# Kernel tuning notes

Hardware: AMD Instinct MI355X
Metric: run time of the kernel (lower is better)

The kernel has to match this reference:

```python
import jax, jax.numpy as jnp
import numpy as np

EPS = 1e-5

def inorm(x, w, b):
    # InstanceNorm1d over token dim (axis=1), per (batch, feature); biased var
    m = x.mean(axis=1, keepdims=True)
    v = ((x - m) ** 2).mean(axis=1, keepdims=True)
    return (x - m) / jnp.sqrt(v + EPS) * w + b

def setup_inputs() -> dict:
    B, N, D, FH = 2, 512, 128, 512
    key = jax.random.key(0)
    ks = iter(jax.random.split(key, 48))
    rn = lambda shape, s=0.05: jax.random.normal(next(ks), shape, jnp.float32) * s
    inp = {
        'row_emb': jax.random.normal(next(ks), (B, N, D), jnp.float32),
        'col_emb': jax.random.normal(next(ks), (B, N, D), jnp.float32),
        'cost_mat': jax.random.uniform(next(ks), (B, N, N), jnp.float32),
        'coords': jax.random.uniform(next(ks), (B, N, 2), jnp.float32),
        'alpha': jnp.ones((1,), jnp.float32),
        # instance norm affine params (weight~1, bias~0)
        'n1_w': 1.0 + rn((D,)), 'n1_b': rn((D,)),
        'n2_w': 1.0 + rn((D,)), 'n2_b': rn((D,)),
        'n3_w': 1.0 + rn((D,)), 'n3_b': rn((D,)),
        'fn1_w': 1.0 + rn((D,)), 'fn1_b': rn((D,)),
        'fn2_w': 1.0 + rn((D,)), 'fn2_b': rn((D,)),
        # AFTFull projections (stored (in,out))
        'q_w': rn((D, D)), 'q_b': rn((D,)),
        'k_w': rn((D, D)), 'k_b': rn((D,)),
        'v_w': rn((D, D)), 'v_b': rn((D,)),
        'p_w': rn((D, D)), 'p_b': rn((D,)),
        'mhc_w': rn((D, D)), 'mhc_b': rn((D,)),
        # DistAngleFusion MLPs
        'dist_w1': rn((1, D)), 'dist_b1': rn((D,)),
        'dist_w2': rn((D, D)), 'dist_b2': rn((D,)),
        'ang_w1': rn((1, D)), 'ang_b1': rn((D,)),
        'ang_w2': rn((D, D)), 'ang_b2': rn((D,)),
        'gate_w': rn((2 * D, 1)), 'gate_b': rn((1,)),
        'outlin_w': rn((D, 1)), 'outlin_b': rn((1,)),
        # FeedForward
        'ffn_w1': rn((D, FH)), 'ffn_b1': rn((FH,)),
        'ffn_w2': rn((FH, D)), 'ffn_b2': rn((D,)),
    }
    return inp

def reference(row_emb, col_emb, cost_mat, coords, alpha,
              n1_w, n1_b, n2_w, n2_b, n3_w, n3_b, fn1_w, fn1_b, fn2_w, fn2_b,
              q_w, q_b, k_w, k_b, v_w, v_b, p_w, p_b, mhc_w, mhc_b,
              dist_w1, dist_b1, dist_w2, dist_b2,
              ang_w1, ang_b1, ang_w2, ang_b2,
              gate_w, gate_b, outlin_w, outlin_b,
              ffn_w1, ffn_b1, ffn_w2, ffn_b2):
    rn = inorm(row_emb, n1_w, n1_b)
    cn = inorm(col_emb, n2_w, n2_b)

    # DistAngleFusion: adapt_bias (B,N,N)
    diff = coords[:, :, None, :] - coords[:, None, :, :]  # (B,N,N,2)
    angles = jnp.arctan2(diff[..., 1], diff[..., 0])
    dist_e = jax.nn.relu(cost_mat[..., None] @ dist_w1 + dist_b1) @ dist_w2 + dist_b2  # (B,N,N,D)
    angle_e = jax.nn.relu(angles[..., None] @ ang_w1 + ang_b1) @ ang_w2 + ang_b2
    g = jax.nn.sigmoid(jnp.concatenate([dist_e, angle_e], axis=-1) @ gate_w + gate_b)  # (B,N,N,1)
    fused = g * dist_e + (1.0 - g) * angle_e
    adapt_bias = (fused @ outlin_w + outlin_b)[..., 0] * alpha  # (B,N,N)

    # AFTFull
    Q = jax.nn.sigmoid(rn @ q_w + q_b)          # (B,N,H)
    K = jax.nn.softmax(cn @ k_w + k_b, axis=1)  # softmax over tokens
    V = cn @ v_w + v_b
    eab = jnp.exp(jax.nn.softmax(adapt_bias, axis=-1))  # (B,N,N)
    eK = jnp.exp(K)
    num = jnp.einsum('bnm,bmh->bnh', eab, eK * V)
    den = jnp.einsum('bnm,bmh->bnh', eab, eK)
    Yt = (Q * (num / den)) @ p_w + p_b

    mh = inorm(Yt @ mhc_w + mhc_b, n3_w, n3_b)

    # TransformerFFN with instance norms
    x = inorm(rn + mh, fn1_w, fn1_b)
    ff = jax.nn.relu(x @ ffn_w1 + ffn_b1) @ ffn_w2 + ffn_b2
    return inorm(x + ff, fn2_w, fn2_b)
```

## Files before the change

### kernel.cpp

```cpp
#include <hip/hip_runtime.h>
#include <hip/hip_bf16.h>
#include <math.h>

#define Bn  2
#define Nn  512
#define Dn  128
#define FHn 512

#define PI_F 3.14159265358979323846f

typedef __hip_bfloat16 bf16;

__device__ __forceinline__ float cvt(float x) { return x; }
__device__ __forceinline__ float cvt(bf16 x) { return __bfloat162float(x); }
__device__ __forceinline__ float sigmoidf_(float x) { return 1.0f / (1.0f + __expf(-x)); }
__device__ __forceinline__ bool is_bf16(const void* alpha) {
    return ((const unsigned short*)alpha)[0] == 0x3F80;
}

__device__ __forceinline__ float fatan2f(float dy, float dx) {
    float ax = fabsf(dx), ay = fabsf(dy);
    float mx = fmaxf(ax, ay), mn = fminf(ax, ay);
    float r = __fdividef(mn, mx);
    float t = r * r;
    float a = r * (0.99997726f + t * (-0.33262347f + t * (0.19354346f +
              t * (-0.11643287f + t * (0.05265332f + t * (-0.01172120f))))));
    if (ay > ax) a = 1.57079632679489662f - a;
    if (dx < 0.f) a = PI_F - a;
    if (dy < 0.f) a = -a;
    return fminf(fmaxf(a, -PI_F), PI_F);
}

#define S_ 131072
#define WS_Q    (0 * S_)
#define WS_K    (1 * S_)
#define WS_V    (2 * S_)
#define WS_EK   (3 * S_)
#define WS_EKV  (4 * S_)
#define WS_EAB  (5 * S_)
#define WS_MH   (1 * S_)
#define WS_T    (2 * S_)
#define WS_OP   (3 * S_)
#define WS_ST   (9 * S_)

#define ST_IN_SC   0
#define ST_IN_SH   512
#define ST_X_SC    2048
#define ST_X_SH    2304
#define ST_PRE     3072
#define P_SC       1024
#define ST_TAB     4224
#define TAB_ANG 644
#define TAB_N   1288
#define ST_LUTC (ST_TAB + TAB_N)
#define ST_LUTA (ST_LUTC + 257)
#define TABLUT_N (TAB_N + 514)

#define SMEM_FLOATS 2568

struct KP {
    const void *row, *col, *cost, *coords, *alpha;
    const void *n1w, *n1b, *n2w, *n2b, *n3w, *n3b, *f1w, *f1b, *f2w, *f2b;
    const void *qw, *qb, *kw, *kb, *vw, *vb, *pw, *pb, *mw, *mb;
    const void *dw1, *db1, *dw2, *db2, *aw1, *ab1, *aw2, *ab2, *gw, *gb, *ow, *ob;
    const void *ffw1, *ffb1, *ffw2, *ffb2;
    void* out;
    float* ws;
};

__device__ __forceinline__ void blk_sum2(float& s, float& ss, volatile float* scr) {
#pragma unroll
    for (int off = 32; off > 0; off >>= 1) { s += __shfl_down(s, off); ss += __shfl_down(ss, off); }
    __syncthreads();
    int wave = threadIdx.x >> 6, lane = threadIdx.x & 63;
    if (lane == 0) { scr[wave] = s; scr[4 + wave] = ss; }
    __syncthreads();
    s = scr[0] + scr[1] + scr[2] + scr[3];
    ss = scr[4] + scr[5] + scr[6] + scr[7];
}

__device__ __forceinline__ float blk_sum1(float v, volatile float* scr) {
#pragma unroll
    for (int off = 32; off > 0; off >>= 1) v += __shfl_down(v, off);
    __syncthreads();
    int wave = threadIdx.x >> 6, lane = threadIdx.x & 63;
    if (lane == 0) scr[wave] = v;
    __syncthreads();
    return scr[0] + scr[1] + scr[2] + scr[3];
}

__device__ __forceinline__ float blk_max1(float v, volatile float* scr) {
#pragma unroll
    for (int off = 32; off > 0; off >>= 1) v = fmaxf(v, __shfl_down(v, off));
    __syncthreads();
    int wave = threadIdx.x >> 6, lane = threadIdx.x & 63;
    if (lane == 0) scr[wave] = v;
    __syncthreads();
    return fmaxf(fmaxf(scr[0], scr[1]), fmaxf(scr[2], scr[3]));
}

template <typename T>
__device__ void build_tables(const T* w1p, const T* b1p, const T* w2p,
                             const T* owp, const T* gwp, float* gtab, float* smem) {
    int tid = threadIdx.x;
    float* W  = smem;
    float* Bb = smem + 128;
    float* U  = smem + 256;
    float* Vv = smem + 384;
    float* Tt = smem + 512;
    int* RK   = (int*)(smem + 640);
    float* STl = smem + 768;
    if (tid < 128) {
        float u = 0.f, v = 0.f;
#pragma unroll 4
        for (int d = 0; d < Dn; ++d) {
            float w2 = cvt(w2p[tid * Dn + d]);
            u += w2 * cvt(owp[d]);
            v += w2 * cvt(gwp[d]);
        }
        float w = cvt(w1p[tid]), b = cvt(b1p[tid]);
        U[tid] = u; Vv[tid] = v; W[tid] = w; Bb[tid] = b;
        Tt[tid] = (w != 0.f) ? (-b / w) : 3.0e38f;
    }
    __syncthreads();
    if (tid < 128) {
        float tk = Tt[tid]; int r = 0;
        for (int j = 0; j < 128; ++j) {
            float tj = Tt[j];
            r += (tj < tk) || (tj == tk && j < tid);
        }
        RK[tid] = r;
        gtab[r] = tk;
        STl[r] = tk;
    }
    __syncthreads();
    if (tid <= 128) {
        int si = tid;
        float slS = 0, inS = 0, slT = 0, inT = 0;
        for (int k = 0; k < 128; ++k) {
            float w = W[k];
            if (w == 0.f) {
                float rb = fmaxf(Bb[k], 0.f);
                inS += rb * U[k];
                inT += rb * Vv[k];
            } else {
                bool act = (w > 0.f) ? (RK[k] < si) : (RK[k] >= si);
                if (act) {
                    slS += w * U[k];  inS += Bb[k] * U[k];
                    slT += w * Vv[k]; inT += Bb[k] * Vv[k];
                }
            }
        }
        gtab[128 + si] = slS;
        gtab[257 + si] = inS;
        gtab[386 + si] = slT;
        gtab[515 + si] = inT;
    }
}

__device__ __forceinline__ int bsearch128(const float* T, float c) {
    int lo = 0, hi = 128;
    while (lo < hi) { int mid = (lo + hi) >> 1; if (T[mid] <= c) lo = mid + 1; else hi = mid; }
    return lo;
}

template <typename T>
__device__ void phase0(const KP& p, float* st, float* smem) {
    float* scr = smem + 2560;
    int cid = blockIdx.x;
    int tid = threadIdx.x;
    {
        int which = cid >> 8, b = (cid >> 7) & 1, d = cid & 127;
        const T* src = (const T*)(which ? p.col : p.row) + (size_t)b * Nn * Dn + d;
        float x0 = cvt(src[(size_t)tid * Dn]);
        float x1 = cvt(src[(size_t)(tid + 256) * Dn]);
        float s = x0 + x1, ss = x0 * x0 + x1 * x1;
        blk_sum2(s, ss, scr);
        if (tid == 0) {
            float m = s * (1.f / Nn);
            float v = fmaxf(ss * (1.f / Nn) - m * m, 0.f);
            float rstd = rsqrtf(v + 1e-5f);
            const T* w = which ? (const T*)p.n2w : (const T*)p.n1w;
            const T* bb = which ? (const T*)p.n2b : (const T*)p.n1b;
            float sc = rstd * cvt(w[d]);
            st[ST_IN_SC + cid] = sc;
            st[ST_IN_SH + cid] = cvt(bb[d]) - m * sc;
        }
    }
    __syncthreads();
    if (cid == 128) {
        const T* db2 = (const T*)p.db2; const T* ab2 = (const T*)p.ab2;
        const T* ow = (const T*)p.ow;   const T* gw = (const T*)p.gw;
        float d2 = 0.f, a2 = 0.f, o = 0.f, g0 = 0.f, g1 = 0.f;
        if (tid < 128) {
            d2 = cvt(db2[tid]); a2 = cvt(ab2[tid]);
            o = cvt(ow[tid]); g0 = cvt(gw[tid]); g1 = cvt(gw[Dn + tid]);
        }
        float cds = d2 * o, cdt = d2 * g0, cas = a2 * o, cat = a2 * g1;
        blk_sum2(cds, cdt, scr);
        blk_sum2(cas, cat, scr);
        if (tid == 0) {
            float* pre = st + ST_PRE;
            pre[P_SC + 0] = cds; pre[P_SC + 1] = cdt;
            pre[P_SC + 2] = cas; pre[P_SC + 3] = cat;
            pre[P_SC + 4] = cvt(((const T*)p.gb)[0]);
            pre[P_SC + 5] = cvt(((const T*)p.ob)[0]);
            pre[P_SC + 6] = cvt(((const T*)p.alpha)[0]);
        }
    } else if (cid == 129) {
        build_tables<T>((const T*)p.dw1, (const T*)p.db1, (const T*)p.dw2,
                        (const T*)p.ow, (const T*)p.gw, st + ST_TAB, smem);
        __syncthreads();
        const float* STl = smem + 768;
        for (int e = tid; e < 257; e += 256) {
            float c = e * (1.f / 256.f);
            st[ST_LUTC + e] = (float)bsearch128(STl, c);
        }
    } else if (cid == 130) {
        build_tables<T>((const T*)p.aw1, (const T*)p.ab1, (const T*)p.aw2,
                        (const T*)p.ow, (const T*)p.gw + Dn, st + ST_TAB + TAB_ANG, smem);
        __syncthreads();
        const float* STl = smem + 768;
        for (int e = tid; e < 257; e += 256) {
            float a = -PI_F + e * (PI_F / 128.f);
            st[ST_LUTA + e] = (float)bsearch128(STl, a);
        }
    }
}

template <typename T>
__device__ void phase1(const KP& p, float* st, float* smem) {
    int tid = threadIdx.x;
    int r0 = blockIdx.x * 2;
    int b = r0 >> 9;
    const T* row = (const T*)p.row; const T* col = (const T*)p.col;
    float* ws = p.ws;
    float* Q = ws + WS_Q; float* Kraw = ws + WS_K; float* V = ws + WS_V;

    float* lr = smem;
    float* lc = smem + 256;
    float* redq = smem + 512;
    float* redk = smem + 1024;
    float* redv = smem + 1536;
    {
        int r = tid >> 7, d = tid & 127;
        float scR = st[ST_IN_SC + b * 128 + d],       shR = st[ST_IN_SH + b * 128 + d];
        float scC = st[ST_IN_SC + 256 + b * 128 + d], shC = st[ST_IN_SH + 256 + b * 128 + d];
        lr[r * 128 + d] = cvt(row[(size_t)(r0 + r) * Dn + d]) * scR + shR;
        lc[r * 128 + d] = cvt(col[(size_t)(r0 + r) * Dn + d]) * scC + shC;
    }
    __syncthreads();
    {
        int h = tid & 127, half = tid >> 7;
        const T* qw = (const T*)p.qw; const T* kw = (const T*)p.kw; const T* vw = (const T*)p.vw;
        float q0 = 0, q1 = 0, ka = 0, kb_ = 0, v0 = 0, v1 = 0;
        int ks = half * 64;
#pragma unroll 8
        for (int k = ks; k < ks + 64; ++k) {
            float wq = cvt(qw[k * Dn + h]);
            float wk = cvt(kw[k * Dn + h]);
            float wv = cvt(vw[k * Dn + h]);
            q0 += lr[k] * wq;        q1 += lr[128 + k] * wq;
            ka += lc[k] * wk;        kb_ += lc[128 + k] * wk;
            v0 += lc[k] * wv;        v1 += lc[128 + k] * wv;
        }
        redq[half * 256 + h] = q0;  redq[half * 256 + 128 + h] = q1;
        redk[half * 256 + h] = ka;  redk[half * 256 + 128 + h] = kb_;
        redv[half * 256 + h] = v0;  redv[half * 256 + 128 + h] = v1;
    }
    __syncthreads();
    if (tid < 128) {
        int h = tid;
        float bq = cvt(((const T*)p.qb)[h]);
        float bk = cvt(((const T*)p.kb)[h]);
        float bv = cvt(((const T*)p.vb)[h]);
#pragma unroll
        for (int r = 0; r < 2; ++r) {
            Q[(r0 + r) * Dn + h]    = sigmoidf_(redq[r * 128 + h] + redq[256 + r * 128 + h] + bq);
            Kraw[(r0 + r) * Dn + h] = redk[r * 128 + h] + redk[256 + r * 128 + h] + bk;
            V[(r0 + r) * Dn + h]    = redv[r * 128 + h] + redv[256 + r * 128 + h] + bv;
        }
    }
    __syncthreads();

    float* tab  = smem;
    float* lutc = smem + 1288;
    float* luta = smem + 1545;
    float* scr  = smem + 1824;
    const float* gt = st + ST_TAB;
    for (int e = tid; e < TABLUT_N; e += 256) smem[e] = gt[e];
    __syncthreads();
    float* eab = ws + WS_EAB;
    const float* pre = st + ST_PRE;
    float cds = pre[P_SC + 0], cdt = pre[P_SC + 1], cas = pre[P_SC + 2], cat = pre[P_SC + 3];
    float gbias = pre[P_SC + 4], obias = pre[P_SC + 5], alpha = pre[P_SC + 6];
    const T* cost = (const T*)p.cost;
    const T* coords = (const T*)p.coords;
    const float* tabA = tab + TAB_ANG;

    float av[2][2];
#pragma unroll
    for (int rr = 0; rr < 2; ++rr) {
        int rowi = r0 + rr;
        int i = rowi & 511;
        float cix = cvt(coords[((size_t)b * Nn + i) * 2 + 0]);
        float ciy = cvt(coords[((size_t)b * Nn + i) * 2 + 1]);
        const T* crow = cost + (size_t)b * Nn * Nn + (size_t)i * Nn;
#pragma unroll
        for (int jj = 0; jj < 2; ++jj) {
            int j = tid + jj * 256;
            float c = cvt(crow[j]);
            int k = (int)(c * 256.f); k = k < 0 ? 0 : (k > 255 ? 255 : k);
            int lo = (int)lutc[k], hi = (int)lutc[k + 1];
            while (lo < hi && tab[lo] <= c) ++lo;
            float sd = fmaf(tab[128 + lo], c, tab[257 + lo]) + cds;
            float td = fmaf(tab[386 + lo], c, tab[515 + lo]) + cdt;
            float dx = cix - cvt(coords[((size_t)b * Nn + j) * 2 + 0]);
            float dy = ciy - cvt(coords[((size_t)b * Nn + j) * 2 + 1]);
            float ang = (dx == 0.f && dy == 0.f) ? 0.f : fatan2f(dy, dx);
            int ka = (int)((ang + PI_F) * (128.f / PI_F)); ka = ka < 0 ? 0 : (ka > 255 ? 255 : ka);
            int la = (int)luta[ka], ha = (int)luta[ka + 1];
            while (la < ha && tabA[la] <= ang) ++la;
            float sa = fmaf(tabA[128 + la], ang, tabA[257 + la]) + cas;
            float ta = fmaf(tabA[386 + la], ang, tabA[515 + la]) + cat;
            float gv = sigmoidf_(td + ta + gbias);
            av[rr][jj] = alpha * (gv * sd + (1.f - gv) * sa + obias);
        }
    }
    int wave = tid >> 6, lane = tid & 63;
    float m0 = fmaxf(av[0][0], av[0][1]);
    float m1 = fmaxf(av[1][0], av[1][1]);
#pragma unroll
    for (int off = 32; off > 0; off >>= 1) {
        m0 = fmaxf(m0, __shfl_down(m0, off));
        m1 = fmaxf(m1, __shfl_down(m1, off));
    }
    if (lane == 0) { scr[wave] = m0; scr[4 + wave] = m1; }
    __syncthreads();
    float mx0 = fmaxf(fmaxf(scr[0], scr[1]), fmaxf(scr[2], scr[3]));
    float mx1 = fmaxf(fmaxf(scr[4], scr[5]), fmaxf(scr[6], scr[7]));
    float e00 = __expf(av[0][0] - mx0), e01 = __expf(av[0][1] - mx0);
    float e10 = __expf(av[1][0] - mx1), e11 = __expf(av[1][1] - mx1);
    float s0 = e00 + e01, s1 = e10 + e11;
#pragma unroll
    for (int off = 32; off > 0; off >>= 1) {
        s0 += __shfl_down(s0, off);
        s1 += __shfl_down(s1, off);
    }
    if (lane == 0) { scr[8 + wave] = s0; scr[12 + wave] = s1; }
    __syncthreads();
    float rs0 = 1.f / (scr[8] + scr[9] + scr[10] + scr[11]);
    float rs1 = 1.f / (scr[12] + scr[13] + scr[14] + scr[15]);
    float* o0 = eab + (size_t)r0 * Nn;
    float* o1 = eab + (size_t)(r0 + 1) * Nn;
    o0[tid] = __expf(e00 * rs0);  o0[tid + 256] = __expf(e01 * rs0);
    o1[tid] = __expf(e10 * rs1);  o1[tid + 256] = __expf(e11 * rs1);
}

__device__ void phase2(const KP& p, float* smem) {
    float* scr = smem + 2560;
    int tid = threadIdx.x;
    int c = blockIdx.x;
    int b = c >> 7, h = c & 127;
    float* ws = p.ws;
    const float* Kraw = ws + WS_K;
    const float* V = ws + WS_V;
    float* eK = ws + WS_EK;
    float* eKV = ws + WS_EKV;
    const float* kb = Kraw + (size_t)b * Nn * Dn + h;
    const float* vb = V + (size_t)b * Nn * Dn + h;
    float x0 = kb[(size_t)tid * Dn];
    float x1 = kb[(size_t)(tid + 256) * Dn];
    float mx = blk_max1(fmaxf(x0, x1), scr);
    float e0 = __expf(x0 - mx), e1 = __expf(x1 - mx);
    float s = blk_sum1(e0 + e1, scr);
    float rs = 1.f / s;
    size_t a0 = (size_t)b * Nn * Dn + (size_t)tid * Dn + h;
    size_t a1 = (size_t)b * Nn * Dn + (size_t)(tid + 256) * Dn + h;
    float ek0 = __expf(e0 * rs), ek1 = __expf(e1 * rs);
    eK[a0] = ek0;  eKV[a0] = ek0 * vb[(size_t)tid * Dn];
    eK[a1] = ek1;  eKV[a1] = ek1 * vb[(size_t)(tid + 256) * Dn];
}

template <typename T>
__device__ void phase3(const KP& p, float* smem) {
    int tid = threadIdx.x;
    int r0 = blockIdx.x * 4;
    int b = r0 >> 9;
    float* ws = p.ws;
    const float* eab = ws + WS_EAB;
    const float* eK = ws + WS_EK;
    const float* eKV = ws + WS_EKV;
    const float* Q = ws + WS_Q;
    float* mh = ws + WS_MH;

    float* ab   = smem;
    float* redn = smem + 2048;
    float* redd = smem + 4096;
    float* gl   = smem + 6144;
    float* yl   = smem + 6656;

    {
        float4* ab4 = (float4*)ab;
        const float4* g4 = (const float4*)(eab + (size_t)r0 * Nn);
        ab4[tid] = g4[tid];
    }
    __syncthreads();
    int h = tid & 127, q = tid >> 7;
    {
        float num[4] = {0,0,0,0}, den[4] = {0,0,0,0};
        int j0 = q * 128;
        const float* ekb = eK + (size_t)b * Nn * Dn + h;
        const float* evb = eKV + (size_t)b * Nn * Dn + h;
#pragma unroll 4
        for (int j = j0; j < j0 + 128; ++j) {
            float ek = ekb[(size_t)j * Dn];
            float ev = evb[(size_t)j * Dn];
#pragma unroll
            for (int r = 0; r < 4; ++r) {
                num[r] += ab[r * 512 + j] * ev;
                den[r] += ab[r * 512 + j] * ek;
            }
        }
#pragma unroll
        for (int r = 0; r < 4; ++r) {
            redn[q * 512 + r * 128 + h] = num[r];
            redd[q * 512 + r * 128 + h] = den[r];
        }
    }
    __syncthreads();
    if (tid < 128) {
#pragma unroll
        for (int r = 0; r < 4; ++r) {
            float nu = redn[r * 128 + h] + redn[512 + r * 128 + h]
                     + redn[1024 + r * 128 + h] + redn[1536 + r * 128 + h];
            float de = redd[r * 128 + h] + redd[512 + r * 128 + h]
                     + redd[1024 + r * 128 + h] + redd[1536 + r * 128 + h];
            gl[r * 128 + h] = Q[(r0 + r) * Dn + h] * nu / de;
        }
    }
    __syncthreads();
    {
        const T* pw = (const T*)p.pw;
        float acc[4] = {0,0,0,0};
        int ks = q * 32;
#pragma unroll 8
        for (int k = ks; k < ks + 32; ++k) {
            float w = cvt(pw[k * Dn + h]);
#pragma unroll
            for (int r = 0; r < 4; ++r) acc[r] += gl[r * 128 + k] * w;
        }
#pragma unroll
        for (int r = 0; r < 4; ++r) redn[q * 512 + r * 128 + h] = acc[r];
    }
    __syncthreads();
    if (tid < 128) {
        float bp = cvt(((const T*)p.pb)[h]);
#pragma unroll
        for (int r = 0; r < 4; ++r)
            yl[r * 128 + h] = redn[r * 128 + h] + redn[512 + r * 128 + h]
                            + redn[1024 + r * 128 + h] + redn[1536 + r * 128 + h] + bp;
    }
    __syncthreads();
    {
        const T* mw = (const T*)p.mw;
        float acc[4] = {0,0,0,0};
        int ks = q * 32;
#pragma unroll 8
        for (int k = ks; k < ks + 32; ++k) {
            float w = cvt(mw[k * Dn + h]);
#pragma unroll
            for (int r = 0; r < 4; ++r) acc[r] += yl[r * 128 + k] * w;
        }
#pragma unroll
        for (int r = 0; r < 4; ++r) redn[q * 512 + r * 128 + h] = acc[r];
    }
    __syncthreads();
    if (tid < 128) {
        float bm = cvt(((const T*)p.mb)[h]);
#pragma unroll
        for (int r = 0; r < 4; ++r)
            mh[(r0 + r) * Dn + h] = redn[r * 128 + h] + redn[512 + r * 128 + h]
                                  + redn[1024 + r * 128 + h] + redn[1536 + r * 128 + h] + bm;
    }
}

template <typename T>
__device__ void phase45(const KP& p, float* st, float* smem) {
    float* scr = smem + 2560;
    int tid = threadIdx.x;
    int c = blockIdx.x;
    int b = c >> 7, d = c & 127;
    const float* mh = p.ws + WS_MH;
    const float* mp = mh + (size_t)b * Nn * Dn + d;
    float m0 = mp[(size_t)tid * Dn], m1 = mp[(size_t)(tid + 256) * Dn];
    float s = m0 + m1, ss = m0 * m0 + m1 * m1;
    blk_sum2(s, ss, scr);
    float mm = s * (1.f / Nn);
    float vv = fmaxf(ss * (1.f / Nn) - mm * mm, 0.f);
    float rstd = rsqrtf(vv + 1e-5f);
    float scM = rstd * cvt(((const T*)p.n3w)[d]);
    float shM = cvt(((const T*)p.n3b)[d]) - mm * scM;
    const T* row = (const T*)p.row;
    float scI = st[ST_IN_SC + c], shI = st[ST_IN_SH + c];
    const T* rp = row + (size_t)b * Nn * Dn + d;
    float* tp = p.ws + WS_T + (size_t)b * Nn * Dn + d;
    float x0 = cvt(rp[(size_t)tid * Dn]) * scI + shI + m0 * scM + shM;
    float x1 = cvt(rp[(size_t)(tid + 256) * Dn]) * scI + shI + m1 * scM + shM;
    tp[(size_t)tid * Dn] = x0;
    tp[(size_t)(tid + 256) * Dn] = x1;
    __syncthreads();
    float s2 = x0 + x1, ss2 = x0 * x0 + x1 * x1;
    blk_sum2(s2, ss2, scr);
    if (tid == 0) {
        float m = s2 * (1.f / Nn);
        float v = fmaxf(ss2 * (1.f / Nn) - m * m, 0.f);
        float r = rsqrtf(v + 1e-5f);
        float sc = r * cvt(((const T*)p.f1w)[d]);
        st[ST_X_SC + c] = sc;
        st[ST_X_SH + c] = cvt(((const T*)p.f1b)[d]) - m * sc;
    }
}

template <typename T>
__device__ void phase6(const KP& p, float* st, float* smem) {
    int tid = threadIdx.x;
    int r0 = blockIdx.x * 4;
    int b = r0 >> 9;
    const float* t = p.ws + WS_T;
    float* outpre = p.ws + WS_OP;
    const T* w1 = (const T*)p.ffw1; const T* b1 = (const T*)p.ffb1;
    const T* w2 = (const T*)p.ffw2; const T* b2 = (const T*)p.ffb2;

    float* xl = smem;
    float* hl = smem + 512;
    float* red = smem + 2560;
    {
        int r = tid >> 7, d = tid & 127;
        int c = b * 128 + d;
        xl[r * 128 + d] = t[(r0 + r) * Dn + d] * st[ST_X_SC + c] + st[ST_X_SH + c];
    }
    __syncthreads();
    {
        int f = tid;
        float a[4] = {0,0,0,0};
#pragma unroll 4
        for (int k = 0; k < Dn; ++k) {
            float w = cvt(w1[k * FHn + f]);
#pragma unroll
            for (int r = 0; r < 4; ++r) a[r] += xl[r * 128 + k] * w;
        }
        float bb1 = cvt(b1[f]);
#pragma unroll
        for (int r = 0; r < 4; ++r) hl[r * 512 + f] = fmaxf(a[r] + bb1, 0.f);
    }
    __syncthreads();
    {
        int d = tid & 127, q = tid >> 7;
        int k0 = q * 128;
        float a[4] = {0,0,0,0};
#pragma unroll 8
        for (int k = k0; k < k0 + 128; ++k) {
            float w = cvt(w2[k * Dn + d]);
#pragma unroll
            for (int r = 0; r < 4; ++r) a[r] += hl[r * 512 + k] * w;
        }
#pragma unroll
        for (int r = 0; r < 4; ++r) red[q * 512 + r * 128 + d] = a[r];
    }
    __syncthreads();
    if (tid < 128) {
        float bb2 = cvt(b2[tid]);
#pragma unroll
        for (int r = 0; r < 4; ++r) {
            float sum = red[r * 128 + tid] + red[512 + r * 128 + tid]
                      + red[1024 + r * 128 + tid] + red[1536 + r * 128 + tid];
            outpre[(r0 + r) * Dn + tid] = xl[r * 128 + tid] + sum + bb2;
        }
    }
}

template <typename T>
__device__ void phase78(const KP& p, float* smem) {
    float* scr = smem + 2560;
    int tid = threadIdx.x;
    int c = blockIdx.x;
    int b = c >> 7, d = c & 127;
    const float* op = p.ws + WS_OP;
    const float* sp = op + (size_t)b * Nn * Dn + d;
    float x0 = sp[(size_t)tid * Dn], x1 = sp[(size_t)(tid + 256) * Dn];
    float s = x0 + x1, ss = x0 * x0 + x1 * x1;
    blk_sum2(s, ss, scr);
    float m = s * (1.f / Nn);
    float v = fmaxf(ss * (1.f / Nn) - m * m, 0.f);
    float rstd = rsqrtf(v + 1e-5f);
    float sc = rstd * cvt(((const T*)p.f2w)[d]);
    float sh = cvt(((const T*)p.f2b)[d]) - m * sc;
    T* out = (T*)p.out + (size_t)b * Nn * Dn + d;
    out[(size_t)tid * Dn] = (T)(x0 * sc + sh);
    out[(size_t)(tid + 256) * Dn] = (T)(x1 * sc + sh);
}

#define PH_WRAP(name, call_bf, call_f)                                        \
__global__ __launch_bounds__(256) void name(KP p) {                           \
    __shared__ float smem[SMEM_FLOATS];                                       \
    float* st = p.ws + WS_ST; (void)st;                                       \
    if (is_bf16(p.alpha)) { call_bf; } else { call_f; }                       \
}

PH_WRAP(k_head,  phase0<bf16>(p, st, smem),  phase0<float>(p, st, smem))
PH_WRAP(k_qkveab, phase1<bf16>(p, st, smem), phase1<float>(p, st, smem))
__global__ __launch_bounds__(256) void k_kekv(KP p) {
    __shared__ float smem[SMEM_FLOATS];
    phase2(p, smem);
}
__global__ __launch_bounds__(512) void k_attn(KP p) {
    __shared__ float smem[7168];
    if (is_bf16(p.alpha)) phase3<bf16>(p, smem);
    else                  phase3<float>(p, smem);
}
PH_WRAP(k_mid,   phase45<bf16>(p, st, smem), phase45<float>(p, st, smem))
__global__ __launch_bounds__(512) void k_ffn(KP p) {
    __shared__ float smem[4608];
    float* st = p.ws + WS_ST;
    if (is_bf16(p.alpha)) phase6<bf16>(p, st, smem);
    else                  phase6<float>(p, st, smem);
}
PH_WRAP(k_tail,  phase78<bf16>(p, smem),     phase78<float>(p, smem))

extern "C" void kernel_launch(void* const* d_in, const int* in_sizes, int n_in,
                              void* d_out, int out_size, void* d_ws, size_t ws_size,
                              hipStream_t stream) {
    KP p;
    p.row = d_in[0];  p.col = d_in[1];  p.cost = d_in[2];  p.coords = d_in[3];
    p.alpha = d_in[4];
    p.n1w = d_in[5];  p.n1b = d_in[6];  p.n2w = d_in[7];  p.n2b = d_in[8];
    p.n3w = d_in[9];  p.n3b = d_in[10]; p.f1w = d_in[11]; p.f1b = d_in[12];
    p.f2w = d_in[13]; p.f2b = d_in[14];
    p.qw = d_in[15];  p.qb = d_in[16];  p.kw = d_in[17];  p.kb = d_in[18];
    p.vw = d_in[19];  p.vb = d_in[20];  p.pw = d_in[21];  p.pb = d_in[22];
    p.mw = d_in[23];  p.mb = d_in[24];
    p.dw1 = d_in[25]; p.db1 = d_in[26]; p.dw2 = d_in[27]; p.db2 = d_in[28];
    p.aw1 = d_in[29]; p.ab1 = d_in[30]; p.aw2 = d_in[31]; p.ab2 = d_in[32];
    p.gw = d_in[33];  p.gb = d_in[34];  p.ow = d_in[35];  p.ob = d_in[36];
    p.ffw1 = d_in[37]; p.ffb1 = d_in[38]; p.ffw2 = d_in[39]; p.ffb2 = d_in[40];
    p.out = d_out;
    p.ws = (float*)d_ws;

    k_head<<<512, 256, 0, stream>>>(p);
    k_qkveab<<<512, 256, 0, stream>>>(p);
    k_kekv<<<256, 256, 0, stream>>>(p);
    k_attn<<<256, 512, 0, stream>>>(p);
    k_mid<<<256, 256, 0, stream>>>(p);
    k_ffn<<<256, 512, 0, stream>>>(p);
    k_tail<<<256, 256, 0, stream>>>(p);
}
```

Baseline: 241.4 us.

## Fuse adaptive-bias softmax and K softmax into attention kernel, drop kekv pass

The adaptive-bias softmax (eab) now runs inside the attention kernel, and the column softmax of K is recomputed there, with exp(K)·V formed on the fly. This removes the separate k_kekv launch and the global round trips for the eab, eK and eKV buffers. The QKV projection moves to 512-thread blocks that handle 4 rows each, which halves its grid and matches the attention tiling. The cost is that every attention block redundantly recomputes the per-column max and sum of K over all 512 tokens, and makes extra passes over K plus extra exp calls.

```diff
diff --git a/kernel.cpp b/kernel.cpp
--- a/kernel.cpp
+++ b/kernel.cpp
@@ -35,13 +35,10 @@
 #define WS_Q    (0 * S_)
 #define WS_K    (1 * S_)
 #define WS_V    (2 * S_)
-#define WS_EK   (3 * S_)
-#define WS_EKV  (4 * S_)
-#define WS_EAB  (5 * S_)
-#define WS_MH   (1 * S_)
-#define WS_T    (2 * S_)
-#define WS_OP   (3 * S_)
-#define WS_ST   (9 * S_)
+#define WS_MH   (3 * S_)
+#define WS_T    (4 * S_)
+#define WS_OP   (5 * S_)
+#define WS_ST   (6 * S_)
 
 #define ST_IN_SC   0
 #define ST_IN_SH   512
@@ -77,26 +74,6 @@
     __syncthreads();
     s = scr[0] + scr[1] + scr[2] + scr[3];
     ss = scr[4] + scr[5] + scr[6] + scr[7];
-}
-
-__device__ __forceinline__ float blk_sum1(float v, volatile float* scr) {
-#pragma unroll
-    for (int off = 32; off > 0; off >>= 1) v += __shfl_down(v, off);
-    __syncthreads();
-    int wave = threadIdx.x >> 6, lane = threadIdx.x & 63;
-    if (lane == 0) scr[wave] = v;
-    __syncthreads();
-    return scr[0] + scr[1] + scr[2] + scr[3];
-}
-
-__device__ __forceinline__ float blk_max1(float v, volatile float* scr) {
-#pragma unroll
-    for (int off = 32; off > 0; off >>= 1) v = fmaxf(v, __shfl_down(v, off));
-    __syncthreads();
-    int wave = threadIdx.x >> 6, lane = threadIdx.x & 63;
-    if (lane == 0) scr[wave] = v;
-    __syncthreads();
-    return fmaxf(fmaxf(scr[0], scr[1]), fmaxf(scr[2], scr[3]));
 }
 
 template <typename T>
@@ -231,17 +208,17 @@
 template <typename T>
 __device__ void phase1(const KP& p, float* st, float* smem) {
     int tid = threadIdx.x;
-    int r0 = blockIdx.x * 2;
+    int r0 = blockIdx.x * 4;
     int b = r0 >> 9;
     const T* row = (const T*)p.row; const T* col = (const T*)p.col;
     float* ws = p.ws;
     float* Q = ws + WS_Q; float* Kraw = ws + WS_K; float* V = ws + WS_V;
 
     float* lr = smem;
-    float* lc = smem + 256;
-    float* redq = smem + 512;
-    float* redk = smem + 1024;
-    float* redv = smem + 1536;
+    float* lc = smem + 512;
+    float* redq = smem + 1024;
+    float* redk = smem + 3072;
+    float* redv = smem + 5120;
     {
         int r = tid >> 7, d = tid & 127;
         float scR = st[ST_IN_SC + b * 128 + d],       shR = st[ST_IN_SH + b * 128 + d];
@@ -251,22 +228,28 @@
     }
     __syncthreads();
     {
-        int h = tid & 127, half = tid >> 7;
+        int h = tid & 127, q = tid >> 7;
         const T* qw = (const T*)p.qw; const T* kw = (const T*)p.kw; const T* vw = (const T*)p.vw;
-        float q0 = 0, q1 = 0, ka = 0, kb_ = 0, v0 = 0, v1 = 0;
-        int ks = half * 64;
+        float aq[4] = {0,0,0,0}, ak[4] = {0,0,0,0}, av[4] = {0,0,0,0};
+        int ks = q * 32;
 #pragma unroll 8
-        for (int k = ks; k < ks + 64; ++k) {
+        for (int k = ks; k < ks + 32; ++k) {
             float wq = cvt(qw[k * Dn + h]);
             float wk = cvt(kw[k * Dn + h]);
             float wv = cvt(vw[k * Dn + h]);
-            q0 += lr[k] * wq;        q1 += lr[128 + k] * wq;
-            ka += lc[k] * wk;        kb_ += lc[128 + k] * wk;
-            v0 += lc[k] * wv;        v1 += lc[128 + k] * wv;
-        }
-        redq[half * 256 + h] = q0;  redq[half * 256 + 128 + h] = q1;
-        redk[half * 256 + h] = ka;  redk[half * 256 + 128 + h] = kb_;
-        redv[half * 256 + h] = v0;  redv[half * 256 + 128 + h] = v1;
+#pragma unroll
+            for (int r = 0; r < 4; ++r) {
+                aq[r] += lr[r * 128 + k] * wq;
+                ak[r] += lc[r * 128 + k] * wk;
+                av[r] += lc[r * 128 + k] * wv;
+            }
+        }
+#pragma unroll
+        for (int r = 0; r < 4; ++r) {
+            redq[q * 512 + r * 128 + h] = aq[r];
+            redk[q * 512 + r * 128 + h] = ak[r];
+            redv[q * 512 + r * 128 + h] = av[r];
+        }
     }
     __syncthreads();
     if (tid < 128) {
@@ -275,48 +258,66 @@
         float bk = cvt(((const T*)p.kb)[h]);
         float bv = cvt(((const T*)p.vb)[h]);
 #pragma unroll
-        for (int r = 0; r < 2; ++r) {
-            Q[(r0 + r) * Dn + h]    = sigmoidf_(redq[r * 128 + h] + redq[256 + r * 128 + h] + bq);
-            Kraw[(r0 + r) * Dn + h] = redk[r * 128 + h] + redk[256 + r * 128 + h] + bk;
-            V[(r0 + r) * Dn + h]    = redv[r * 128 + h] + redv[256 + r * 128 + h] + bv;
-        }
-    }
-    __syncthreads();
-
-    float* tab  = smem;
-    float* lutc = smem + 1288;
-    float* luta = smem + 1545;
-    float* scr  = smem + 1824;
-    const float* gt = st + ST_TAB;
-    for (int e = tid; e < TABLUT_N; e += 256) smem[e] = gt[e];
-    __syncthreads();
-    float* eab = ws + WS_EAB;
-    const float* pre = st + ST_PRE;
-    float cds = pre[P_SC + 0], cdt = pre[P_SC + 1], cas = pre[P_SC + 2], cat = pre[P_SC + 3];
-    float gbias = pre[P_SC + 4], obias = pre[P_SC + 5], alpha = pre[P_SC + 6];
-    const T* cost = (const T*)p.cost;
-    const T* coords = (const T*)p.coords;
-    const float* tabA = tab + TAB_ANG;
-
-    float av[2][2];
-#pragma unroll
-    for (int rr = 0; rr < 2; ++rr) {
-        int rowi = r0 + rr;
-        int i = rowi & 511;
-        float cix = cvt(coords[((size_t)b * Nn + i) * 2 + 0]);
-        float ciy = cvt(coords[((size_t)b * Nn + i) * 2 + 1]);
-        const T* crow = cost + (size_t)b * Nn * Nn + (size_t)i * Nn;
-#pragma unroll
-        for (int jj = 0; jj < 2; ++jj) {
-            int j = tid + jj * 256;
-            float c = cvt(crow[j]);
+        for (int r = 0; r < 4; ++r) {
+            float qv = redq[r*128+h] + redq[512 + r*128+h] + redq[1024 + r*128+h] + redq[1536 + r*128+h] + bq;
+            float kv = redk[r*128+h] + redk[512 + r*128+h] + redk[1024 + r*128+h] + redk[1536 + r*128+h] + bk;
+            float vv = redv[r*128+h] + redv[512 + r*128+h] + redv[1024 + r*128+h] + redv[1536 + r*128+h] + bv;
+            Q[(r0 + r) * Dn + h]    = sigmoidf_(qv);
+            Kraw[(r0 + r) * Dn + h] = kv;
+            V[(r0 + r) * Dn + h]    = vv;
+        }
+    }
+}
+
+template <typename T>
+__device__ void phase3(const KP& p, float* st, float* smem) {
+    int tid = threadIdx.x;
+    int r0 = blockIdx.x * 4;
+    int b = r0 >> 9;
+    float* ws = p.ws;
+    const float* Kraw = ws + WS_K;
+    const float* V = ws + WS_V;
+    const float* Q = ws + WS_Q;
+    float* mh = ws + WS_MH;
+
+    float* ab   = smem;
+    float* redn = smem + 2048;
+    float* redd = smem + 4096;
+    float* gl   = smem + 6144;
+    float* yl   = smem + 6656;
+    float* scr  = smem + 7168;
+
+    {
+        float* tab  = smem + 2048;
+        float* lutc = smem + 3336;
+        float* luta = smem + 3593;
+        const float* gt = st + ST_TAB;
+        for (int e = tid; e < TABLUT_N; e += 512) tab[e] = gt[e];
+        __syncthreads();
+        const float* pre = st + ST_PRE;
+        float cds = pre[P_SC + 0], cdt = pre[P_SC + 1], cas = pre[P_SC + 2], cat = pre[P_SC + 3];
+        float gbias = pre[P_SC + 4], obias = pre[P_SC + 5], alpha = pre[P_SC + 6];
+        const T* cost = (const T*)p.cost;
+        const T* coords = (const T*)p.coords;
+        const float* tabA = tab + TAB_ANG;
+
+        int j = tid;
+        float cjx = cvt(coords[((size_t)b * Nn + j) * 2 + 0]);
+        float cjy = cvt(coords[((size_t)b * Nn + j) * 2 + 1]);
+        float av[4];
+#pragma unroll
+        for (int rr = 0; rr < 4; ++rr) {
+            int i = (r0 + rr) & 511;
+            float cix = cvt(coords[((size_t)b * Nn + i) * 2 + 0]);
+            float ciy = cvt(coords[((size_t)b * Nn + i) * 2 + 1]);
+            float c = cvt(cost[(size_t)b * Nn * Nn + (size_t)i * Nn + j]);
             int k = (int)(c * 256.f); k = k < 0 ? 0 : (k > 255 ? 255 : k);
             int lo = (int)lutc[k], hi = (int)lutc[k + 1];
             while (lo < hi && tab[lo] <= c) ++lo;
             float sd = fmaf(tab[128 + lo], c, tab[257 + lo]) + cds;
             float td = fmaf(tab[386 + lo], c, tab[515 + lo]) + cdt;
-            float dx = cix - cvt(coords[((size_t)b * Nn + j) * 2 + 0]);
-            float dy = ciy - cvt(coords[((size_t)b * Nn + j) * 2 + 1]);
+            float dx = cix - cjx;
+            float dy = ciy - cjy;
             float ang = (dx == 0.f && dy == 0.f) ? 0.f : fatan2f(dy, dx);
             int ka = (int)((ang + PI_F) * (128.f / PI_F)); ka = ka < 0 ? 0 : (ka > 255 ? 255 : ka);
             int la = (int)luta[ka], ha = (int)luta[ka + 1];
@@ -324,101 +325,79 @@
             float sa = fmaf(tabA[128 + la], ang, tabA[257 + la]) + cas;
             float ta = fmaf(tabA[386 + la], ang, tabA[515 + la]) + cat;
             float gv = sigmoidf_(td + ta + gbias);
-            av[rr][jj] = alpha * (gv * sd + (1.f - gv) * sa + obias);
-        }
-    }
-    int wave = tid >> 6, lane = tid & 63;
-    float m0 = fmaxf(av[0][0], av[0][1]);
-    float m1 = fmaxf(av[1][0], av[1][1]);
-#pragma unroll
-    for (int off = 32; off > 0; off >>= 1) {
-        m0 = fmaxf(m0, __shfl_down(m0, off));
-        m1 = fmaxf(m1, __shfl_down(m1, off));
-    }
-    if (lane == 0) { scr[wave] = m0; scr[4 + wave] = m1; }
-    __syncthreads();
-    float mx0 = fmaxf(fmaxf(scr[0], scr[1]), fmaxf(scr[2], scr[3]));
-    float mx1 = fmaxf(fmaxf(scr[4], scr[5]), fmaxf(scr[6], scr[7]));
-    float e00 = __expf(av[0][0] - mx0), e01 = __expf(av[0][1] - mx0);
-    float e10 = __expf(av[1][0] - mx1), e11 = __expf(av[1][1] - mx1);
-    float s0 = e00 + e01, s1 = e10 + e11;
-#pragma unroll
-    for (int off = 32; off > 0; off >>= 1) {
-        s0 += __shfl_down(s0, off);
-        s1 += __shfl_down(s1, off);
-    }
-    if (lane == 0) { scr[8 + wave] = s0; scr[12 + wave] = s1; }
-    __syncthreads();
-    float rs0 = 1.f / (scr[8] + scr[9] + scr[10] + scr[11]);
-    float rs1 = 1.f / (scr[12] + scr[13] + scr[14] + scr[15]);
-    float* o0 = eab + (size_t)r0 * Nn;
-    float* o1 = eab + (size_t)(r0 + 1) * Nn;
-    o0[tid] = __expf(e00 * rs0);  o0[tid + 256] = __expf(e01 * rs0);
-    o1[tid] = __expf(e10 * rs1);  o1[tid + 256] = __expf(e11 * rs1);
-}
-
-__device__ void phase2(const KP& p, float* smem) {
-    float* scr = smem + 2560;
-    int tid = threadIdx.x;
-    int c = blockIdx.x;
-    int b = c >> 7, h = c & 127;
-    float* ws = p.ws;
-    const float* Kraw = ws + WS_K;
-    const float* V = ws + WS_V;
-    float* eK = ws + WS_EK;
-    float* eKV = ws + WS_EKV;
-    const float* kb = Kraw + (size_t)b * Nn * Dn + h;
-    const float* vb = V + (size_t)b * Nn * Dn + h;
-    float x0 = kb[(size_t)tid * Dn];
-    float x1 = kb[(size_t)(tid + 256) * Dn];
-    float mx = blk_max1(fmaxf(x0, x1), scr);
-    float e0 = __expf(x0 - mx), e1 = __expf(x1 - mx);
-    float s = blk_sum1(e0 + e1, scr);
-    float rs = 1.f / s;
-    size_t a0 = (size_t)b * Nn * Dn + (size_t)tid * Dn + h;
-    size_t a1 = (size_t)b * Nn * Dn + (size_t)(tid + 256) * Dn + h;
-    float ek0 = __expf(e0 * rs), ek1 = __expf(e1 * rs);
-    eK[a0] = ek0;  eKV[a0] = ek0 * vb[(size_t)tid * Dn];
-    eK[a1] = ek1;  eKV[a1] = ek1 * vb[(size_t)(tid + 256) * Dn];
-}
-
-template <typename T>
-__device__ void phase3(const KP& p, float* smem) {
-    int tid = threadIdx.x;
-    int r0 = blockIdx.x * 4;
-    int b = r0 >> 9;
-    float* ws = p.ws;
-    const float* eab = ws + WS_EAB;
-    const float* eK = ws + WS_EK;
-    const float* eKV = ws + WS_EKV;
-    const float* Q = ws + WS_Q;
-    float* mh = ws + WS_MH;
-
-    float* ab   = smem;
-    float* redn = smem + 2048;
-    float* redd = smem + 4096;
-    float* gl   = smem + 6144;
-    float* yl   = smem + 6656;
-
-    {
-        float4* ab4 = (float4*)ab;
-        const float4* g4 = (const float4*)(eab + (size_t)r0 * Nn);
-        ab4[tid] = g4[tid];
-    }
-    __syncthreads();
+            av[rr] = alpha * (gv * sd + (1.f - gv) * sa + obias);
+        }
+        int wave = tid >> 6, lane = tid & 63;
+        float t0 = av[0], t1 = av[1], t2 = av[2], t3 = av[3];
+#pragma unroll
+        for (int off = 32; off > 0; off >>= 1) {
+            t0 = fmaxf(t0, __shfl_down(t0, off));
+            t1 = fmaxf(t1, __shfl_down(t1, off));
+            t2 = fmaxf(t2, __shfl_down(t2, off));
+            t3 = fmaxf(t3, __shfl_down(t3, off));
+        }
+        __syncthreads();
+        if (lane == 0) { scr[wave] = t0; scr[8 + wave] = t1; scr[16 + wave] = t2; scr[24 + wave] = t3; }
+        __syncthreads();
+        float mx[4], ev[4];
+#pragma unroll
+        for (int rr = 0; rr < 4; ++rr) {
+            float m = scr[rr * 8];
+#pragma unroll
+            for (int w = 1; w < 8; ++w) m = fmaxf(m, scr[rr * 8 + w]);
+            mx[rr] = m;
+            ev[rr] = __expf(av[rr] - m);
+        }
+        float s0 = ev[0], s1 = ev[1], s2 = ev[2], s3 = ev[3];
+#pragma unroll
+        for (int off = 32; off > 0; off >>= 1) {
+            s0 += __shfl_down(s0, off);
+            s1 += __shfl_down(s1, off);
+            s2 += __shfl_down(s2, off);
+            s3 += __shfl_down(s3, off);
+        }
+        if (lane == 0) { scr[32 + wave] = s0; scr[40 + wave] = s1; scr[48 + wave] = s2; scr[56 + wave] = s3; }
+        __syncthreads();
+#pragma unroll
+        for (int rr = 0; rr < 4; ++rr) {
+            float s = 0.f;
+#pragma unroll
+            for (int w = 0; w < 8; ++w) s += scr[32 + rr * 8 + w];
+            ab[rr * 512 + j] = __expf(ev[rr] / s);
+        }
+    }
+    __syncthreads();
+
     int h = tid & 127, q = tid >> 7;
+    const float* kbase = Kraw + (size_t)b * Nn * Dn + h;
+    const float* vbase = V + (size_t)b * Nn * Dn + h;
+    int j0 = q * 128;
+
+    float mxk, rsk;
+    {
+        float lm = -3.0e38f;
+        for (int j = j0; j < j0 + 128; ++j) lm = fmaxf(lm, kbase[(size_t)j * Dn]);
+        redn[q * 128 + h] = lm;
+        __syncthreads();
+        mxk = fmaxf(fmaxf(redn[h], redn[128 + h]), fmaxf(redn[256 + h], redn[384 + h]));
+        float ls = 0.f;
+        for (int j = j0; j < j0 + 128; ++j) ls += __expf(kbase[(size_t)j * Dn] - mxk);
+        redd[q * 128 + h] = ls;
+        __syncthreads();
+        rsk = 1.f / (redd[h] + redd[128 + h] + redd[256 + h] + redd[384 + h]);
+    }
+    __syncthreads();
+
     {
         float num[4] = {0,0,0,0}, den[4] = {0,0,0,0};
-        int j0 = q * 128;
-        const float* ekb = eK + (size_t)b * Nn * Dn + h;
-        const float* evb = eKV + (size_t)b * Nn * Dn + h;
 #pragma unroll 4
         for (int j = j0; j < j0 + 128; ++j) {
-            float ek = ekb[(size_t)j * Dn];
-            float ev = evb[(size_t)j * Dn];
+            float kv_ = kbase[(size_t)j * Dn];
+            float ek = __expf(__expf(kv_ - mxk) * rsk);
+            float ev_ = ek * vbase[(size_t)j * Dn];
 #pragma unroll
             for (int r = 0; r < 4; ++r) {
-                num[r] += ab[r * 512 + j] * ev;
+                num[r] += ab[r * 512 + j] * ev_;
                 den[r] += ab[r * 512 + j] * ek;
             }
         }
@@ -609,15 +588,17 @@
 }
 
 PH_WRAP(k_head,  phase0<bf16>(p, st, smem),  phase0<float>(p, st, smem))
-PH_WRAP(k_qkveab, phase1<bf16>(p, st, smem), phase1<float>(p, st, smem))
-__global__ __launch_bounds__(256) void k_kekv(KP p) {
-    __shared__ float smem[SMEM_FLOATS];
-    phase2(p, smem);
+__global__ __launch_bounds__(512) void k_qkv(KP p) {
+    __shared__ float smem[7168];
+    float* st = p.ws + WS_ST;
+    if (is_bf16(p.alpha)) phase1<bf16>(p, st, smem);
+    else                  phase1<float>(p, st, smem);
 }
 __global__ __launch_bounds__(512) void k_attn(KP p) {
-    __shared__ float smem[7168];
-    if (is_bf16(p.alpha)) phase3<bf16>(p, smem);
-    else                  phase3<float>(p, smem);
+    __shared__ float smem[7232];
+    float* st = p.ws + WS_ST;
+    if (is_bf16(p.alpha)) phase3<bf16>(p, st, smem);
+    else                  phase3<float>(p, st, smem);
 }
 PH_WRAP(k_mid,   phase45<bf16>(p, st, smem), phase45<float>(p, st, smem))
 __global__ __launch_bounds__(512) void k_ffn(KP p) {
@@ -648,8 +629,7 @@
     p.ws = (float*)d_ws;
 
     k_head<<<512, 256, 0, stream>>>(p);
-    k_qkveab<<<512, 256, 0, stream>>>(p);
-    k_kekv<<<256, 256, 0, stream>>>(p);
+    k_qkv<<<256, 512, 0, stream>>>(p);
     k_attn<<<256, 512, 0, stream>>>(p);
     k_mid<<<256, 256, 0, stream>>>(p);
     k_ffn<<<256, 512, 0, stream>>>(p);
```

Result: slower. 253.3 us (+4.9%).
